# Kernel tuning notes

Hardware: AMD Instinct MI355X
Metric: run time of the kernel (lower is better)

## Reference

```python
import jax, jax.numpy as jnp
import numpy as np

N_NODES = 100000
N_EDGES = 1600000
D_IN = 64
D_HID = 64
D_ACT = 16


def gcn_conv(x, W, b, src, dst, n_nodes):
    """PyG-style GCNConv: D^-1/2 (A+I) D^-1/2 (x @ W) + b."""
    h = x @ W  # [N, out]
    ones = jnp.ones(src.shape[0], dtype=x.dtype)
    # degree with self-loops (in-degree + 1)
    deg = jax.ops.segment_sum(ones, dst, num_segments=n_nodes) + 1.0
    dinv = jax.lax.rsqrt(deg)  # [N]
    coef = dinv[src] * dinv[dst]  # [E]
    agg = jax.ops.segment_sum(h[src] * coef[:, None], dst, num_segments=n_nodes)
    agg = agg + h * (dinv * dinv)[:, None]  # self-loop term
    return agg + b


def setup_inputs() -> dict:
    key = jax.random.key(0)
    ks = jax.random.split(key, 6)
    x = jax.random.normal(ks[0], (N_NODES, D_IN), dtype=jnp.float32)
    edge_index = jax.random.randint(ks[1], (2, N_EDGES), 0, N_NODES, dtype=jnp.int64)
    s1 = 1.0 / np.sqrt(D_IN)
    s2 = 1.0 / np.sqrt(D_HID)
    W1 = jax.random.normal(ks[2], (D_IN, D_HID), dtype=jnp.float32) * s1
    b1 = jnp.zeros((D_HID,), dtype=jnp.float32)
    W2 = jax.random.normal(ks[3], (D_HID, D_HID), dtype=jnp.float32) * s2
    b2 = jnp.zeros((D_HID,), dtype=jnp.float32)
    Wfc = jax.random.normal(ks[4], (D_HID, D_ACT), dtype=jnp.float32) * s2
    bfc = jnp.zeros((D_ACT,), dtype=jnp.float32)
    return {"x": x, "edge_index": edge_index, "W1": W1, "b1": b1,
            "W2": W2, "b2": b2, "Wfc": Wfc, "bfc": bfc}


def reference(x, edge_index, W1, b1, W2, b2, Wfc, bfc):
    src, dst = edge_index[0], edge_index[1]
    n = x.shape[0]
    h = jax.nn.relu(gcn_conv(x, W1, b1, src, dst, n))
    h = jax.nn.relu(gcn_conv(h, W2, b2, src, dst, n))
    q_values = h @ Wfc + bfc
    return q_values
```

## Files before the change

kernel.cpp:

```cpp
#include <hip/hip_runtime.h>

#define NN 100000
#define NE 1600000
#define NCAP 64
#define NB 391
#define NBK 512
#define CAPG 768
#define CHUNK 2048
#define NCHUNK 782

typedef __attribute__((ext_vector_type(8))) short short8;
typedef __attribute__((ext_vector_type(4))) float f32x4;

static __device__ __forceinline__ unsigned short f2bf(float f) {
    unsigned u = __float_as_uint(f);
    u += 0x7fffu + ((u >> 16) & 1u);
    return (unsigned short)(u >> 16);
}
static __device__ __forceinline__ float bflo(unsigned u) { return __uint_as_float(u << 16); }
static __device__ __forceinline__ float bfhi(unsigned u) { return __uint_as_float(u & 0xffff0000u); }

static __device__ __forceinline__ short8 as_s8(uint4 u) {
    union { uint4 u4; short8 s8; } x; x.u4 = u; return x.s8;
}
static __device__ __forceinline__ f32x4 mfma16(short8 a, short8 b, f32x4 c) {
    return __builtin_amdgcn_mfma_f32_16x16x32_bf16(a, b, c, 0, 0, 0);
}

static __device__ __forceinline__ void split8(float4 a, float4 b, short8& hi8, short8& lo8) {
    float vv[8] = {a.x, a.y, a.z, a.w, b.x, b.y, b.z, b.w};
    unsigned h[8], l[8];
    #pragma unroll
    for (int j = 0; j < 8; ++j) {
        h[j] = f2bf(vv[j]);
        l[j] = f2bf(vv[j] - bflo(h[j]));
    }
    uint4 uh, ul;
    uh.x = h[0] | (h[1] << 16); uh.y = h[2] | (h[3] << 16);
    uh.z = h[4] | (h[5] << 16); uh.w = h[6] | (h[7] << 16);
    ul.x = l[0] | (l[1] << 16); ul.y = l[2] | (l[3] << 16);
    ul.z = l[4] | (l[5] << 16); ul.w = l[6] | (l[7] << 16);
    hi8 = as_s8(uh); lo8 = as_s8(ul);
}

__global__ __launch_bounds__(256) void bin_edges(const int* __restrict__ src,
                                                 const int* __restrict__ dst,
                                                 int* __restrict__ gcur,
                                                 int* __restrict__ pairs) {
    __shared__ int lcnt[NBK];
    __shared__ int lnext[NBK];
    int t = threadIdx.x;
    int grp = blockIdx.x & 7;
    lcnt[t] = 0; lcnt[t + 256] = 0;
    __syncthreads();
    int base = blockIdx.x * CHUNK;
    int sr[8], dr[8];
    #pragma unroll
    for (int i = 0; i < 8; ++i) {
        int e = base + t + 256 * i;
        bool v = e < NE;
        sr[i] = v ? src[e] : 0;
        dr[i] = v ? dst[e] : -1;
        if (v) atomicAdd(&lcnt[dr[i] >> 8], 1);
    }
    __syncthreads();
    #pragma unroll
    for (int i = 0; i < 2; ++i) {
        int b = t + 256 * i;
        int v = lcnt[b];
        if (v) lnext[b] = ((grp << 9) + b) * CAPG + atomicAdd(&gcur[(grp << 9) + b], v);
    }
    __syncthreads();
    #pragma unroll
    for (int i = 0; i < 8; ++i) {
        if (dr[i] >= 0) {
            int p = atomicAdd(&lnext[dr[i] >> 8], 1);
            pairs[p] = sr[i] | ((dr[i] & 255) << 17);
        }
    }
}

__global__ __launch_bounds__(256) void slab_gemm1(const int* __restrict__ pairs,
                                                  const int* __restrict__ gcur,
                                                  const float* __restrict__ X,
                                                  const uint4* __restrict__ WP,
                                                  int* __restrict__ esrc,
                                                  int* __restrict__ cnt,
                                                  float* __restrict__ dinv,
                                                  uint4* __restrict__ G4) {
    __shared__ int lc[256];
    __shared__ float ldv[256];
    __shared__ __align__(16) unsigned short Ls[4][16][64];
    int b = blockIdx.x;
    int t = threadIdx.x;
    lc[t] = 0;
    __syncthreads();
    #pragma unroll
    for (int g = 0; g < 8; ++g) {
        int rid = (g << 9) + b;
        int e0 = rid * CAPG;
        int n = min(gcur[rid], CAPG);
        for (int i0 = t * 4; i0 < n; i0 += 1024) {
            int4 w4 = *(const int4*)&pairs[e0 + i0];
            int wv[4] = {w4.x, w4.y, w4.z, w4.w};
            #pragma unroll
            for (int k = 0; k < 4; ++k) {
                if (i0 + k < n) {
                    int w = wv[k];
                    int li = w >> 17;
                    int p = atomicAdd(&lc[li], 1);
                    if (p < NCAP - 1) esrc[(((b << 8) + li) << 6) + p] = w & 0x1FFFF;
                }
            }
        }
    }
    __syncthreads();
    {
        int node = (b << 8) + t;
        if (node < NN) {
            int c = lc[t];
            int cc = min(c, NCAP - 1);
            esrc[(node << 6) + cc] = node;
            cnt[node] = cc + 1;
            float dv = rsqrtf((float)c + 1.0f);
            dinv[node] = dv;
            ldv[t] = dv;
        }
    }
    __syncthreads();

    int wave = t >> 6, lane = t & 63;
    int r = lane & 15, g = lane >> 4;
    #pragma unroll
    for (int ti = 0; ti < 4; ++ti) {
        int T = wave * 4 + ti;
        int node0 = (b << 8) + T * 16;
        if (node0 < NN) {
            const float* xr = X + (size_t)(node0 + r) * 64 + g * 8;
            float4 x0a = *(const float4*)(xr);
            float4 x0b = *(const float4*)(xr + 4);
            float4 x1a = *(const float4*)(xr + 32);
            float4 x1b = *(const float4*)(xr + 36);
            short8 ah0, al0, ah1, al1;
            split8(x0a, x0b, ah0, al0);
            split8(x1a, x1b, ah1, al1);
            f32x4 acc[4];
            #pragma unroll
            for (int c = 0; c < 4; ++c) acc[c] = (f32x4){0.f, 0.f, 0.f, 0.f};
            #pragma unroll
            for (int c = 0; c < 4; ++c) {
                short8 bh0 = as_s8(WP[(c * 2 + 0) * 64 + lane]);
                short8 bl0 = as_s8(WP[512 + (c * 2 + 0) * 64 + lane]);
                short8 bh1 = as_s8(WP[(c * 2 + 1) * 64 + lane]);
                short8 bl1 = as_s8(WP[512 + (c * 2 + 1) * 64 + lane]);
                acc[c] = mfma16(ah0, bh0, acc[c]);
                acc[c] = mfma16(al0, bh0, acc[c]);
                acc[c] = mfma16(ah0, bl0, acc[c]);
                acc[c] = mfma16(ah1, bh1, acc[c]);
                acc[c] = mfma16(al1, bh1, acc[c]);
                acc[c] = mfma16(ah1, bl1, acc[c]);
            }
            float dd[4];
            #pragma unroll
            for (int rr = 0; rr < 4; ++rr) dd[rr] = ldv[T * 16 + g * 4 + rr];
            #pragma unroll
            for (int c = 0; c < 4; ++c) {
                #pragma unroll
                for (int rr = 0; rr < 4; ++rr)
                    Ls[wave][g * 4 + rr][c * 16 + r] = f2bf(acc[c][rr] * dd[rr]);
            }
            #pragma unroll
            for (int i = 0; i < 2; ++i) {
                int idx = lane + i * 64;
                int row = idx >> 3, u = idx & 7;
                G4[(size_t)(node0 + row) * 8 + u] = *(const uint4*)&Ls[wave][row][u * 8];
            }
        }
    }
}

__global__ void wpack(const float* __restrict__ W1, const float* __restrict__ W2,
                      uint4* __restrict__ P, int* __restrict__ gcur) {
    int tid = blockIdx.x * blockDim.x + threadIdx.x;
    if (tid >= 1024) return;
    ((uint4*)gcur)[tid] = make_uint4(0, 0, 0, 0);
    int w = tid >> 9;
    int f = tid & 511;
    int c = f >> 7;
    int t = (f >> 6) & 1;
    int lane = f & 63;
    const float* W = w ? W2 : W1;
    int k0 = t * 32 + (lane >> 4) * 8;
    int n  = c * 16 + (lane & 15);
    unsigned sh[8], sl[8];
    #pragma unroll
    for (int j = 0; j < 8; ++j) {
        float v = W[(k0 + j) * 64 + n];
        sh[j] = f2bf(v);
        sl[j] = f2bf(v - bflo(sh[j]));
    }
    uint4 ph, pl;
    ph.x = sh[0] | (sh[1] << 16); ph.y = sh[2] | (sh[3] << 16);
    ph.z = sh[4] | (sh[5] << 16); ph.w = sh[6] | (sh[7] << 16);
    pl.x = sl[0] | (sl[1] << 16); pl.y = sl[2] | (sl[3] << 16);
    pl.z = sl[4] | (sl[5] << 16); pl.w = sl[6] | (sl[7] << 16);
    P[w * 1024 + f]       = ph;
    P[w * 1024 + 512 + f] = pl;
}

__global__ __launch_bounds__(256) void gemm2_mfma(const uint4* __restrict__ X4,
                                                  const uint4* __restrict__ WP,
                                                  const float* __restrict__ dinv,
                                                  uint4* __restrict__ G4) {
    __shared__ __align__(16) unsigned short Ls[4][16][64];
    int wave = threadIdx.x >> 6, lane = threadIdx.x & 63;
    int tile = blockIdx.x * 4 + wave;
    bool active = tile < (NN / 16);
    int node0 = (active ? tile : 0) * 16;
    int r = lane & 15, g = lane >> 4;

    short8 a0 = as_s8(X4[(size_t)(node0 + r) * 8 + g]);
    short8 a1 = as_s8(X4[(size_t)(node0 + r) * 8 + 4 + g]);

    f32x4 acc[4];
    #pragma unroll
    for (int c = 0; c < 4; ++c) acc[c] = (f32x4){0.f, 0.f, 0.f, 0.f};
    #pragma unroll
    for (int c = 0; c < 4; ++c) {
        short8 bh0 = as_s8(WP[(c * 2 + 0) * 64 + lane]);
        short8 bl0 = as_s8(WP[512 + (c * 2 + 0) * 64 + lane]);
        short8 bh1 = as_s8(WP[(c * 2 + 1) * 64 + lane]);
        short8 bl1 = as_s8(WP[512 + (c * 2 + 1) * 64 + lane]);
        acc[c] = mfma16(a0, bh0, acc[c]);
        acc[c] = mfma16(a0, bl0, acc[c]);
        acc[c] = mfma16(a1, bh1, acc[c]);
        acc[c] = mfma16(a1, bl1, acc[c]);
    }
    float dd[4];
    #pragma unroll
    for (int rr = 0; rr < 4; ++rr) dd[rr] = dinv[node0 + g * 4 + rr];
    #pragma unroll
    for (int c = 0; c < 4; ++c) {
        #pragma unroll
        for (int rr = 0; rr < 4; ++rr)
            Ls[wave][g * 4 + rr][c * 16 + r] = f2bf(acc[c][rr] * dd[rr]);
    }
    if (active) {
        #pragma unroll
        for (int i = 0; i < 2; ++i) {
            int idx = lane + i * 64;
            int row = idx >> 3, u = idx & 7;
            G4[(size_t)(node0 + row) * 8 + u] = *(const uint4*)&Ls[wave][row][u * 8];
        }
    }
}

#define ACC8(u) do { \
    a0 += bflo((u).x); a1 += bfhi((u).x); a2 += bflo((u).y); a3 += bfhi((u).y); \
    a4 += bflo((u).z); a5 += bfhi((u).z); a6 += bflo((u).w); a7 += bfhi((u).w); } while (0)

#define GATHER_CORE(node)                                                     \
    int j0 = (node) << 6;                                                     \
    int e1 = j0 + cnt[node];                                                  \
    float a0 = 0.f, a1 = 0.f, a2 = 0.f, a3 = 0.f,                             \
          a4 = 0.f, a5 = 0.f, a6 = 0.f, a7 = 0.f;                             \
    int j = j0 + e;                                                           \
    for (; j + 8 < e1; j += 16) {                                             \
        int s0 = esrc[j], s1 = esrc[j + 8];                                   \
        uint4 u0 = G4[s0 * 8 + m];                                            \
        uint4 u1 = G4[s1 * 8 + m];                                            \
        ACC8(u0); ACC8(u1);                                                   \
    }                                                                         \
    for (; j < e1; j += 8) {                                                  \
        uint4 u = G4[esrc[j] * 8 + m];                                        \
        ACC8(u);                                                              \
    }                                                                         \
    a0 += __shfl_xor(a0, 8);  a1 += __shfl_xor(a1, 8);                        \
    a2 += __shfl_xor(a2, 8);  a3 += __shfl_xor(a3, 8);                        \
    a4 += __shfl_xor(a4, 8);  a5 += __shfl_xor(a5, 8);                        \
    a6 += __shfl_xor(a6, 8);  a7 += __shfl_xor(a7, 8);                        \
    a0 += __shfl_xor(a0, 16); a1 += __shfl_xor(a1, 16);                       \
    a2 += __shfl_xor(a2, 16); a3 += __shfl_xor(a3, 16);                       \
    a4 += __shfl_xor(a4, 16); a5 += __shfl_xor(a5, 16);                       \
    a6 += __shfl_xor(a6, 16); a7 += __shfl_xor(a7, 16);                       \
    a0 += __shfl_xor(a0, 32); a1 += __shfl_xor(a1, 32);                       \
    a2 += __shfl_xor(a2, 32); a3 += __shfl_xor(a3, 32);                       \
    a4 += __shfl_xor(a4, 32); a5 += __shfl_xor(a5, 32);                       \
    a6 += __shfl_xor(a6, 32); a7 += __shfl_xor(a7, 32);

__global__ __launch_bounds__(256) void gather_bf16(
        const int* __restrict__ cnt, const int* __restrict__ esrc,
        const float* __restrict__ dinv, const uint4* __restrict__ G4,
        const float* __restrict__ b, uint4* __restrict__ outH) {
    int node = blockIdx.x * 4 + (threadIdx.x >> 6);
    int lane = threadIdx.x & 63;
    int e = lane >> 3, m = lane & 7;
    GATHER_CORE(node)
    if (e == 0) {
        float dd = dinv[node];
        float4 b0 = ((const float4*)b)[2 * m];
        float4 b1v = ((const float4*)b)[2 * m + 1];
        float h0 = fmaxf(fmaf(a0, dd, b0.x), 0.f);
        float h1 = fmaxf(fmaf(a1, dd, b0.y), 0.f);
        float h2 = fmaxf(fmaf(a2, dd, b0.z), 0.f);
        float h3 = fmaxf(fmaf(a3, dd, b0.w), 0.f);
        float h4 = fmaxf(fmaf(a4, dd, b1v.x), 0.f);
        float h5 = fmaxf(fmaf(a5, dd, b1v.y), 0.f);
        float h6 = fmaxf(fmaf(a6, dd, b1v.z), 0.f);
        float h7 = fmaxf(fmaf(a7, dd, b1v.w), 0.f);
        uint4 pk;
        pk.x = (unsigned)f2bf(h0) | ((unsigned)f2bf(h1) << 16);
        pk.y = (unsigned)f2bf(h2) | ((unsigned)f2bf(h3) << 16);
        pk.z = (unsigned)f2bf(h4) | ((unsigned)f2bf(h5) << 16);
        pk.w = (unsigned)f2bf(h6) | ((unsigned)f2bf(h7) << 16);
        outH[(size_t)node * 8 + m] = pk;
    }
}

__global__ __launch_bounds__(256) void gather_fc(
        const int* __restrict__ cnt, const int* __restrict__ esrc,
        const float* __restrict__ dinv, const uint4* __restrict__ G4,
        const float* __restrict__ b2, const float* __restrict__ Wfc,
        const float* __restrict__ bfc, float* __restrict__ out) {
    int node = blockIdx.x * 4 + (threadIdx.x >> 6);
    int lane = threadIdx.x & 63;
    int e = lane >> 3, m = lane & 7;
    int q = lane >> 4, c = lane & 15;
    float Wreg[16];
    #pragma unroll
    for (int i = 0; i < 16; ++i) Wreg[i] = Wfc[(q * 16 + i) * 16 + c];
    GATHER_CORE(node)
    float dd = dinv[node];
    float4 b0 = ((const float4*)b2)[2 * m];
    float4 b1v = ((const float4*)b2)[2 * m + 1];
    a0 = fmaxf(fmaf(a0, dd, b0.x), 0.f);
    a1 = fmaxf(fmaf(a1, dd, b0.y), 0.f);
    a2 = fmaxf(fmaf(a2, dd, b0.z), 0.f);
    a3 = fmaxf(fmaf(a3, dd, b0.w), 0.f);
    a4 = fmaxf(fmaf(a4, dd, b1v.x), 0.f);
    a5 = fmaxf(fmaf(a5, dd, b1v.y), 0.f);
    a6 = fmaxf(fmaf(a6, dd, b1v.z), 0.f);
    a7 = fmaxf(fmaf(a7, dd, b1v.w), 0.f);
    int sl0 = 2 * q, sl1 = 2 * q + 1;
    float acc = 0.f;
    acc = fmaf(__shfl(a0, sl0), Wreg[0], acc);
    acc = fmaf(__shfl(a1, sl0), Wreg[1], acc);
    acc = fmaf(__shfl(a2, sl0), Wreg[2], acc);
    acc = fmaf(__shfl(a3, sl0), Wreg[3], acc);
    acc = fmaf(__shfl(a4, sl0), Wreg[4], acc);
    acc = fmaf(__shfl(a5, sl0), Wreg[5], acc);
    acc = fmaf(__shfl(a6, sl0), Wreg[6], acc);
    acc = fmaf(__shfl(a7, sl0), Wreg[7], acc);
    acc = fmaf(__shfl(a0, sl1), Wreg[8], acc);
    acc = fmaf(__shfl(a1, sl1), Wreg[9], acc);
    acc = fmaf(__shfl(a2, sl1), Wreg[10], acc);
    acc = fmaf(__shfl(a3, sl1), Wreg[11], acc);
    acc = fmaf(__shfl(a4, sl1), Wreg[12], acc);
    acc = fmaf(__shfl(a5, sl1), Wreg[13], acc);
    acc = fmaf(__shfl(a6, sl1), Wreg[14], acc);
    acc = fmaf(__shfl(a7, sl1), Wreg[15], acc);
    acc += __shfl_xor(acc, 16);
    acc += __shfl_xor(acc, 32);
    if (lane < 16) out[node * 16 + c] = acc + bfc[c];
}

extern "C" void kernel_launch(void* const* d_in, const int* in_sizes, int n_in,
                              void* d_out, int out_size, void* d_ws, size_t ws_size,
                              hipStream_t stream) {
    const float* x   = (const float*)d_in[0];
    const int*   ei  = (const int*)d_in[1];
    const float* W1  = (const float*)d_in[2];
    const float* b1  = (const float*)d_in[3];
    const float* W2  = (const float*)d_in[4];
    const float* b2  = (const float*)d_in[5];
    const float* Wfc = (const float*)d_in[6];
    const float* bfc = (const float*)d_in[7];
    float* out = (float*)d_out;

    const int* src = ei;
    const int* dst = ei + NE;

    int*      gcur  = (int*)d_ws;
    int*      cnt   = gcur + 4096;
    float*    dinvp = (float*)(cnt + NN);
    int*      esrc  = (int*)(dinvp + NN);
    unsigned* G     = (unsigned*)(esrc + (size_t)NN * NCAP);
    uint4*    bufB  = (uint4*)(G + (size_t)NN * 32);
    uint4*    WPK   = (uint4*)((unsigned*)bufB + (size_t)NN * 32);
    int*      pairs = (int*)bufB;

    wpack<<<4, 256, 0, stream>>>(W1, W2, WPK, gcur);
    bin_edges<<<NCHUNK, 256, 0, stream>>>(src, dst, gcur, pairs);
    slab_gemm1<<<NB, 256, 0, stream>>>(pairs, gcur, x, WPK, esrc, cnt, dinvp, (uint4*)G);

    gather_bf16<<<NN / 4, 256, 0, stream>>>(cnt, esrc, dinvp, (const uint4*)G, b1, bufB);

    gemm2_mfma<<<(NN / 16 + 3) / 4, 256, 0, stream>>>(bufB, WPK + 1024, dinvp, (uint4*)G);
    gather_fc<<<NN / 4, 256, 0, stream>>>(cnt, esrc, dinvp, (const uint4*)G, b2, Wfc, bfc, out);
}
```

Measured before the change: 226.7 us.

## Store features in column-sliced layout and gather per slice for cache locality

Feature matrices are stored as 8 slices of 16 bytes per node, laid out slice-major, instead of row-major. The gathers now run one block per (16-node group, slice), so each block's random reads hit a 1.6 MB slice that fits in cache better. The final FC is split out of the second gather into its own kernel. The cost is that edge indices are re-read 8 times and an extra launch is added.

```diff
diff --git a/kernel.cpp b/kernel.cpp
--- a/kernel.cpp
+++ b/kernel.cpp
@@ -87,7 +87,7 @@
                                                   int* __restrict__ esrc,
                                                   int* __restrict__ cnt,
                                                   float* __restrict__ dinv,
-                                                  uint4* __restrict__ G4) {
+                                                  uint4* __restrict__ G4s) {
     __shared__ int lc[256];
     __shared__ float ldv[256];
     __shared__ __align__(16) unsigned short Ls[4][16][64];
@@ -172,8 +172,8 @@
             #pragma unroll
             for (int i = 0; i < 2; ++i) {
                 int idx = lane + i * 64;
-                int row = idx >> 3, u = idx & 7;
-                G4[(size_t)(node0 + row) * 8 + u] = *(const uint4*)&Ls[wave][row][u * 8];
+                int u = idx >> 4, row = idx & 15;
+                G4s[(size_t)u * NN + node0 + row] = *(const uint4*)&Ls[wave][row][u * 8];
             }
         }
     }
@@ -208,10 +208,10 @@
     P[w * 1024 + 512 + f] = pl;
 }
 
-__global__ __launch_bounds__(256) void gemm2_mfma(const uint4* __restrict__ X4,
+__global__ __launch_bounds__(256) void gemm2_mfma(const uint4* __restrict__ H1s,
                                                   const uint4* __restrict__ WP,
                                                   const float* __restrict__ dinv,
-                                                  uint4* __restrict__ G4) {
+                                                  uint4* __restrict__ G4s) {
     __shared__ __align__(16) unsigned short Ls[4][16][64];
     int wave = threadIdx.x >> 6, lane = threadIdx.x & 63;
     int tile = blockIdx.x * 4 + wave;
@@ -219,8 +219,8 @@
     int node0 = (active ? tile : 0) * 16;
     int r = lane & 15, g = lane >> 4;
 
-    short8 a0 = as_s8(X4[(size_t)(node0 + r) * 8 + g]);
-    short8 a1 = as_s8(X4[(size_t)(node0 + r) * 8 + 4 + g]);
+    short8 a0 = as_s8(H1s[(size_t)g * NN + node0 + r]);
+    short8 a1 = as_s8(H1s[(size_t)(4 + g) * NN + node0 + r]);
 
     f32x4 acc[4];
     #pragma unroll
@@ -249,8 +249,8 @@
         #pragma unroll
         for (int i = 0; i < 2; ++i) {
             int idx = lane + i * 64;
-            int row = idx >> 3, u = idx & 7;
-            G4[(size_t)(node0 + row) * 8 + u] = *(const uint4*)&Ls[wave][row][u * 8];
+            int u = idx >> 4, row = idx & 15;
+            G4s[(size_t)u * NN + node0 + row] = *(const uint4*)&Ls[wave][row][u * 8];
         }
     }
 }
@@ -259,47 +259,36 @@
     a0 += bflo((u).x); a1 += bfhi((u).x); a2 += bflo((u).y); a3 += bfhi((u).y); \
     a4 += bflo((u).z); a5 += bfhi((u).z); a6 += bflo((u).w); a7 += bfhi((u).w); } while (0)
 
-#define GATHER_CORE(node)                                                     \
-    int j0 = (node) << 6;                                                     \
-    int e1 = j0 + cnt[node];                                                  \
-    float a0 = 0.f, a1 = 0.f, a2 = 0.f, a3 = 0.f,                             \
-          a4 = 0.f, a5 = 0.f, a6 = 0.f, a7 = 0.f;                             \
-    int j = j0 + e;                                                           \
-    for (; j + 8 < e1; j += 16) {                                             \
-        int s0 = esrc[j], s1 = esrc[j + 8];                                   \
-        uint4 u0 = G4[s0 * 8 + m];                                            \
-        uint4 u1 = G4[s1 * 8 + m];                                            \
-        ACC8(u0); ACC8(u1);                                                   \
-    }                                                                         \
-    for (; j < e1; j += 8) {                                                  \
-        uint4 u = G4[esrc[j] * 8 + m];                                        \
-        ACC8(u);                                                              \
-    }                                                                         \
-    a0 += __shfl_xor(a0, 8);  a1 += __shfl_xor(a1, 8);                        \
-    a2 += __shfl_xor(a2, 8);  a3 += __shfl_xor(a3, 8);                        \
-    a4 += __shfl_xor(a4, 8);  a5 += __shfl_xor(a5, 8);                        \
-    a6 += __shfl_xor(a6, 8);  a7 += __shfl_xor(a7, 8);                        \
-    a0 += __shfl_xor(a0, 16); a1 += __shfl_xor(a1, 16);                       \
-    a2 += __shfl_xor(a2, 16); a3 += __shfl_xor(a3, 16);                       \
-    a4 += __shfl_xor(a4, 16); a5 += __shfl_xor(a5, 16);                       \
-    a6 += __shfl_xor(a6, 16); a7 += __shfl_xor(a7, 16);                       \
-    a0 += __shfl_xor(a0, 32); a1 += __shfl_xor(a1, 32);                       \
-    a2 += __shfl_xor(a2, 32); a3 += __shfl_xor(a3, 32);                       \
-    a4 += __shfl_xor(a4, 32); a5 += __shfl_xor(a5, 32);                       \
-    a6 += __shfl_xor(a6, 32); a7 += __shfl_xor(a7, 32);
-
-__global__ __launch_bounds__(256) void gather_bf16(
+__global__ __launch_bounds__(256) void gather_slice(
         const int* __restrict__ cnt, const int* __restrict__ esrc,
-        const float* __restrict__ dinv, const uint4* __restrict__ G4,
-        const float* __restrict__ b, uint4* __restrict__ outH) {
-    int node = blockIdx.x * 4 + (threadIdx.x >> 6);
+        const float* __restrict__ dinv, const uint4* __restrict__ Gs,
+        const float* __restrict__ bias, uint4* __restrict__ Hs) {
+    int blk = blockIdx.x;
+    int s = blk & 7;
+    int nblk = blk >> 3;
     int lane = threadIdx.x & 63;
-    int e = lane >> 3, m = lane & 7;
-    GATHER_CORE(node)
-    if (e == 0) {
+    int n = lane >> 4, l = lane & 15;
+    int node = nblk * 16 + (threadIdx.x >> 6) * 4 + n;
+    const uint4* Gb = Gs + (size_t)s * NN;
+    int cn = cnt[node];
+    int base = node << 6;
+    float a0 = 0.f, a1 = 0.f, a2 = 0.f, a3 = 0.f,
+          a4 = 0.f, a5 = 0.f, a6 = 0.f, a7 = 0.f;
+    for (int j = base + l, jend = base + cn; j < jend; j += 16) {
+        uint4 u = Gb[esrc[j]];
+        ACC8(u);
+    }
+    #pragma unroll
+    for (int off = 1; off < 16; off <<= 1) {
+        a0 += __shfl_xor(a0, off); a1 += __shfl_xor(a1, off);
+        a2 += __shfl_xor(a2, off); a3 += __shfl_xor(a3, off);
+        a4 += __shfl_xor(a4, off); a5 += __shfl_xor(a5, off);
+        a6 += __shfl_xor(a6, off); a7 += __shfl_xor(a7, off);
+    }
+    if (l == 0) {
         float dd = dinv[node];
-        float4 b0 = ((const float4*)b)[2 * m];
-        float4 b1v = ((const float4*)b)[2 * m + 1];
+        float4 b0 = ((const float4*)bias)[2 * s];
+        float4 b1v = ((const float4*)bias)[2 * s + 1];
         float h0 = fmaxf(fmaf(a0, dd, b0.x), 0.f);
         float h1 = fmaxf(fmaf(a1, dd, b0.y), 0.f);
         float h2 = fmaxf(fmaf(a2, dd, b0.z), 0.f);
@@ -313,55 +302,46 @@
         pk.y = (unsigned)f2bf(h2) | ((unsigned)f2bf(h3) << 16);
         pk.z = (unsigned)f2bf(h4) | ((unsigned)f2bf(h5) << 16);
         pk.w = (unsigned)f2bf(h6) | ((unsigned)f2bf(h7) << 16);
-        outH[(size_t)node * 8 + m] = pk;
-    }
-}
-
-__global__ __launch_bounds__(256) void gather_fc(
-        const int* __restrict__ cnt, const int* __restrict__ esrc,
-        const float* __restrict__ dinv, const uint4* __restrict__ G4,
-        const float* __restrict__ b2, const float* __restrict__ Wfc,
-        const float* __restrict__ bfc, float* __restrict__ out) {
-    int node = blockIdx.x * 4 + (threadIdx.x >> 6);
-    int lane = threadIdx.x & 63;
-    int e = lane >> 3, m = lane & 7;
+        Hs[(size_t)s * NN + node] = pk;
+    }
+}
+
+__global__ __launch_bounds__(256) void fc_out(const uint4* __restrict__ H2s,
+                                              const float* __restrict__ Wfc,
+                                              const float* __restrict__ bfc,
+                                              float* __restrict__ out) {
+    int wave = threadIdx.x >> 6, lane = threadIdx.x & 63;
     int q = lane >> 4, c = lane & 15;
     float Wreg[16];
     #pragma unroll
     for (int i = 0; i < 16; ++i) Wreg[i] = Wfc[(q * 16 + i) * 16 + c];
-    GATHER_CORE(node)
-    float dd = dinv[node];
-    float4 b0 = ((const float4*)b2)[2 * m];
-    float4 b1v = ((const float4*)b2)[2 * m + 1];
-    a0 = fmaxf(fmaf(a0, dd, b0.x), 0.f);
-    a1 = fmaxf(fmaf(a1, dd, b0.y), 0.f);
-    a2 = fmaxf(fmaf(a2, dd, b0.z), 0.f);
-    a3 = fmaxf(fmaf(a3, dd, b0.w), 0.f);
-    a4 = fmaxf(fmaf(a4, dd, b1v.x), 0.f);
-    a5 = fmaxf(fmaf(a5, dd, b1v.y), 0.f);
-    a6 = fmaxf(fmaf(a6, dd, b1v.z), 0.f);
-    a7 = fmaxf(fmaf(a7, dd, b1v.w), 0.f);
-    int sl0 = 2 * q, sl1 = 2 * q + 1;
-    float acc = 0.f;
-    acc = fmaf(__shfl(a0, sl0), Wreg[0], acc);
-    acc = fmaf(__shfl(a1, sl0), Wreg[1], acc);
-    acc = fmaf(__shfl(a2, sl0), Wreg[2], acc);
-    acc = fmaf(__shfl(a3, sl0), Wreg[3], acc);
-    acc = fmaf(__shfl(a4, sl0), Wreg[4], acc);
-    acc = fmaf(__shfl(a5, sl0), Wreg[5], acc);
-    acc = fmaf(__shfl(a6, sl0), Wreg[6], acc);
-    acc = fmaf(__shfl(a7, sl0), Wreg[7], acc);
-    acc = fmaf(__shfl(a0, sl1), Wreg[8], acc);
-    acc = fmaf(__shfl(a1, sl1), Wreg[9], acc);
-    acc = fmaf(__shfl(a2, sl1), Wreg[10], acc);
-    acc = fmaf(__shfl(a3, sl1), Wreg[11], acc);
-    acc = fmaf(__shfl(a4, sl1), Wreg[12], acc);
-    acc = fmaf(__shfl(a5, sl1), Wreg[13], acc);
-    acc = fmaf(__shfl(a6, sl1), Wreg[14], acc);
-    acc = fmaf(__shfl(a7, sl1), Wreg[15], acc);
-    acc += __shfl_xor(acc, 16);
-    acc += __shfl_xor(acc, 32);
-    if (lane < 16) out[node * 16 + c] = acc + bfc[c];
+    int node0 = (blockIdx.x * 4 + wave) * 4;
+    #pragma unroll
+    for (int nd = 0; nd < 4; ++nd) {
+        int node = node0 + nd;
+        uint4 ua = H2s[(size_t)(2 * q) * NN + node];
+        uint4 ub = H2s[(size_t)(2 * q + 1) * NN + node];
+        float acc = 0.f;
+        acc = fmaf(bflo(ua.x), Wreg[0], acc);
+        acc = fmaf(bfhi(ua.x), Wreg[1], acc);
+        acc = fmaf(bflo(ua.y), Wreg[2], acc);
+        acc = fmaf(bfhi(ua.y), Wreg[3], acc);
+        acc = fmaf(bflo(ua.z), Wreg[4], acc);
+        acc = fmaf(bfhi(ua.z), Wreg[5], acc);
+        acc = fmaf(bflo(ua.w), Wreg[6], acc);
+        acc = fmaf(bfhi(ua.w), Wreg[7], acc);
+        acc = fmaf(bflo(ub.x), Wreg[8], acc);
+        acc = fmaf(bfhi(ub.x), Wreg[9], acc);
+        acc = fmaf(bflo(ub.y), Wreg[10], acc);
+        acc = fmaf(bfhi(ub.y), Wreg[11], acc);
+        acc = fmaf(bflo(ub.z), Wreg[12], acc);
+        acc = fmaf(bfhi(ub.z), Wreg[13], acc);
+        acc = fmaf(bflo(ub.w), Wreg[14], acc);
+        acc = fmaf(bfhi(ub.w), Wreg[15], acc);
+        acc += __shfl_xor(acc, 16);
+        acc += __shfl_xor(acc, 32);
+        if (lane < 16) out[node * 16 + c] = acc + bfc[c];
+    }
 }
 
 extern "C" void kernel_launch(void* const* d_in, const int* in_sizes, int n_in,
@@ -384,17 +364,19 @@
     int*      cnt   = gcur + 4096;
     float*    dinvp = (float*)(cnt + NN);
     int*      esrc  = (int*)(dinvp + NN);
-    unsigned* G     = (unsigned*)(esrc + (size_t)NN * NCAP);
-    uint4*    bufB  = (uint4*)(G + (size_t)NN * 32);
-    uint4*    WPK   = (uint4*)((unsigned*)bufB + (size_t)NN * 32);
-    int*      pairs = (int*)bufB;
+    uint4*    A     = (uint4*)(esrc + (size_t)NN * NCAP);
+    uint4*    B     = A + (size_t)NN * 8;
+    uint4*    WPK   = B + (size_t)NN * 8;
+    int*      pairs = (int*)B;
 
     wpack<<<4, 256, 0, stream>>>(W1, W2, WPK, gcur);
     bin_edges<<<NCHUNK, 256, 0, stream>>>(src, dst, gcur, pairs);
-    slab_gemm1<<<NB, 256, 0, stream>>>(pairs, gcur, x, WPK, esrc, cnt, dinvp, (uint4*)G);
-
-    gather_bf16<<<NN / 4, 256, 0, stream>>>(cnt, esrc, dinvp, (const uint4*)G, b1, bufB);
-
-    gemm2_mfma<<<(NN / 16 + 3) / 4, 256, 0, stream>>>(bufB, WPK + 1024, dinvp, (uint4*)G);
-    gather_fc<<<NN / 4, 256, 0, stream>>>(cnt, esrc, dinvp, (const uint4*)G, b2, Wfc, bfc, out);
-}
+    slab_gemm1<<<NB, 256, 0, stream>>>(pairs, gcur, x, WPK, esrc, cnt, dinvp, A);
+
+    gather_slice<<<(NN / 16) * 8, 256, 0, stream>>>(cnt, esrc, dinvp, A, b1, B);
+
+    gemm2_mfma<<<(NN / 16 + 3) / 4, 256, 0, stream>>>(B, WPK + 1024, dinvp, A);
+    gather_slice<<<(NN / 16) * 8, 256, 0, stream>>>(cnt, esrc, dinvp, A, b2, B);
+
+    fc_out<<<NN / 16, 256, 0, stream>>>(B, Wfc, bfc, out);
+}
```

New measurement: 310.5 us. +37.0%, slower.
